# Performance work log

Hardware: AMD Instinct MI355X
Metric: run time of the kernel (lower is better)

Reference implementation:

```python
import jax, jax.numpy as jnp
import numpy as np

D = 256; NH = 8; NL = 4; NP = 4; DH = D // NH; DFFN = 1024; NQ = 900; BS = 4
SPATIAL = ((92, 92), (46, 46), (23, 23), (12, 12))  # (H, W) per level
LEVEL_START = (0, 8464, 10580, 11109)
S = sum(h * w for h, w in SPATIAL)  # 11253


def _ln(x, g, b):
    m = jnp.mean(x, -1, keepdims=True)
    v = jnp.var(x, -1, keepdims=True)
    return (x - m) / jnp.sqrt(v + 1e-5) * g + b


def setup_inputs() -> dict:
    key = jax.random.key(0)
    ks = jax.random.split(key, 24)
    p = lambda k, s: 0.02 * jax.random.normal(k, s, jnp.float32)
    return {
        "tgt": jax.random.normal(ks[0], (NQ, BS, D), jnp.float32),
        "tgt_query_pos": jax.random.normal(ks[1], (NQ, BS, D), jnp.float32),
        "tgt_reference_points": jax.random.uniform(ks[2], (NQ, BS, NL, 2), jnp.float32),
        "memory": jax.random.normal(ks[3], (S, BS, D), jnp.float32),
        "memory_spatial_shapes": jnp.array(SPATIAL, jnp.int32),
        "memory_level_start_index": jnp.array(LEVEL_START, jnp.int32),
        "in_proj_w": p(ks[4], (3 * D, D)), "in_proj_b": p(ks[5], (3 * D,)),
        "out_proj_w": p(ks[6], (D, D)), "out_proj_b": p(ks[7], (D,)),
        "off_w": p(ks[8], (NH * NL * NP * 2, D)), "off_b": p(ks[9], (NH * NL * NP * 2,)),
        "aw_w": p(ks[10], (NH * NL * NP, D)), "aw_b": p(ks[11], (NH * NL * NP,)),
        "vproj_w": p(ks[12], (D, D)), "vproj_b": p(ks[13], (D,)),
        "oproj_w": p(ks[14], (D, D)), "oproj_b": p(ks[15], (D,)),
        "ln1_g": jnp.ones((D,), jnp.float32), "ln1_b": jnp.zeros((D,), jnp.float32),
        "ln2_g": jnp.ones((D,), jnp.float32), "ln2_b": jnp.zeros((D,), jnp.float32),
        "ln3_g": jnp.ones((D,), jnp.float32), "ln3_b": jnp.zeros((D,), jnp.float32),
        "lin1_w": p(ks[16], (DFFN, D)), "lin1_b": p(ks[17], (DFFN,)),
        "lin2_w": p(ks[18], (D, DFFN)), "lin2_b": p(ks[19], (D,)),
    }


def _self_attn(q, k, v, in_w, in_b, out_w, out_b):
    # q, k, v: (nq, bs, d) -- torch nn.MultiheadAttention, eval mode
    wq, wk, wv = jnp.split(in_w, 3, axis=0)
    bq, bk, bv = jnp.split(in_b, 3)
    qp = (q @ wq.T + bq).reshape(NQ, BS, NH, DH)
    kp = (k @ wk.T + bk).reshape(NQ, BS, NH, DH)
    vp = (v @ wv.T + bv).reshape(NQ, BS, NH, DH)
    s = jnp.einsum("qbhd,kbhd->bhqk", qp, kp) / jnp.sqrt(jnp.float32(DH))
    a = jax.nn.softmax(s, axis=-1)
    o = jnp.einsum("bhqk,kbhd->qbhd", a, vp).reshape(NQ, BS, D)
    return o @ out_w.T + out_b


def _msdeform(x, ref, mem, off_w, off_b, aw_w, aw_b, vproj_w, vproj_b, oproj_w, oproj_b):
    # x: (bs, nq, d); ref: (bs, nq, nl, 2) in [0,1]; mem: (bs, S, d)
    value = (mem @ vproj_w.T + vproj_b).reshape(BS, S, NH, DH)
    off = (x @ off_w.T + off_b).reshape(BS, NQ, NH, NL, NP, 2)
    aw = jax.nn.softmax((x @ aw_w.T + aw_b).reshape(BS, NQ, NH, NL * NP), axis=-1)
    aw = aw.reshape(BS, NQ, NH, NL, NP)
    # offset normalizer = (W, H) per level
    norm = jnp.array([[w, h] for (h, w) in SPATIAL], jnp.float32)
    loc = ref[:, :, None, :, None, :] + off / norm[None, None, None, :, None, :]
    out = jnp.zeros((BS, NH, NQ, DH), x.dtype)
    for l, (H, W) in enumerate(SPATIAL):
        s0 = LEVEL_START[l]
        v = value[:, s0:s0 + H * W].transpose(0, 2, 1, 3)  # (bs, nh, H*W, dh)
        g = loc[:, :, :, l].transpose(0, 2, 1, 3, 4)       # (bs, nh, nq, np, 2)
        # grid_sample align_corners=False, padding_mode='zeros'
        px = g[..., 0] * W - 0.5
        py = g[..., 1] * H - 0.5
        x0 = jnp.floor(px).astype(jnp.int32)
        y0 = jnp.floor(py).astype(jnp.int32)
        wx = px - x0
        wy = py - y0
        samp = jnp.zeros((BS, NH, NQ, NP, DH), x.dtype)
        for dx, dy, w in ((0, 0, (1 - wx) * (1 - wy)), (1, 0, wx * (1 - wy)),
                          (0, 1, (1 - wx) * wy), (1, 1, wx * wy)):
            xi = x0 + dx
            yi = y0 + dy
            valid = ((xi >= 0) & (xi < W) & (yi >= 0) & (yi < H)).astype(x.dtype)
            idx = (jnp.clip(yi, 0, H - 1) * W + jnp.clip(xi, 0, W - 1)).reshape(BS, NH, NQ * NP)
            gat = jnp.take_along_axis(v, idx[..., None], axis=2).reshape(BS, NH, NQ, NP, DH)
            samp = samp + (w * valid)[..., None] * gat
        a = aw[:, :, :, l].transpose(0, 2, 1, 3)  # (bs, nh, nq, np)
        out = out + (samp * a[..., None]).sum(axis=3)
    out = out.transpose(0, 2, 1, 3).reshape(BS, NQ, D)
    return out @ oproj_w.T + oproj_b


def reference(tgt, tgt_query_pos, tgt_reference_points, memory,
              memory_spatial_shapes, memory_level_start_index,
              in_proj_w, in_proj_b, out_proj_w, out_proj_b,
              off_w, off_b, aw_w, aw_b, vproj_w, vproj_b, oproj_w, oproj_b,
              ln1_g, ln1_b, ln2_g, ln2_b, ln3_g, ln3_b,
              lin1_w, lin1_b, lin2_w, lin2_b):
    # module_seq = ['sa', 'ca', 'ffn']; dropout inactive (eval)
    q = tgt + tgt_query_pos
    tgt2 = _self_attn(q, q, tgt, in_proj_w, in_proj_b, out_proj_w, out_proj_b)
    tgt = _ln(tgt + tgt2, ln2_g, ln2_b)
    x = (tgt + tgt_query_pos).transpose(1, 0, 2)
    ref = tgt_reference_points.transpose(1, 0, 2, 3)
    mem = memory.transpose(1, 0, 2)
    tgt2 = _msdeform(x, ref, mem, off_w, off_b, aw_w, aw_b,
                     vproj_w, vproj_b, oproj_w, oproj_b).transpose(1, 0, 2)
    tgt = _ln(tgt + tgt2, ln1_g, ln1_b)
    ff = jax.nn.relu(tgt @ lin1_w.T + lin1_b) @ lin2_w.T + lin2_b
    return _ln(tgt + ff, ln3_g, ln3_b)
```

## Files before the change

### kernel.cpp

```cpp
#include <hip/hip_runtime.h>
#include <math.h>

#define D_MODEL 256
#define NHEAD   8
#define NLVL    4
#define NPTS    4
#define DHEAD   32
#define DFFN    1024
#define NQ      900
#define BSZ     4
#define NROW    (NQ * BSZ)
#define S_TOT   11253
#define VROWS   (S_TOT * BSZ)
#define SASCALE 0.17677669529663687f

typedef __attribute__((ext_vector_type(8))) short short8;
typedef __attribute__((ext_vector_type(4))) float f32x4;
typedef unsigned short ushort_t;

static __device__ __forceinline__ unsigned f2bf1(float f) {
    unsigned u = __float_as_uint(f);
    return (u + 0x7FFFu + ((u >> 16) & 1u)) >> 16;
}
static __device__ __forceinline__ unsigned pack2bf(float x, float y) {
// ... 243 lines not shown
                    const ushort_t* src = &Cs[r * 136 + ch];
                    uint4* dst = (uint4*)(value16 + (size_t)m * 256 + half * 128 + ch);
#pragma unroll
                    for (int j = 0; j < 4; ++j)
                        dst[j] = *(const uint4*)(src + j * 8);
                }
            }
        }
    }
}

__global__ __launch_bounds__(256) void sa_flash16(
    const ushort_t* __restrict__ qkv, ushort_t* __restrict__ attn_out)
{
    __shared__ ushort_t Ks[2 * 2080];
    __shared__ ushort_t Vt[2 * 2304];
    __shared__ ushort_t Ps[4 * 1152];

    const int t    = threadIdx.x;
    const int q0   = blockIdx.x * 64;
    const int b    = blockIdx.y & 3;
    const int h    = blockIdx.y >> 2;
    const int wv   = t >> 6;
    const int ln   = t & 63;
    const int L    = ln & 15;
    const int quad = ln >> 4;

    union { uint4 u; short8 s; } qu;
    qu.u = make_uint4(0u, 0u, 0u, 0u);
    {
        int q = q0 + wv * 16 + L;
        if (q < NQ)
            qu.u = *(const uint4*)(qkv + ((size_t)q * 4 + b) * 768 + h * 32 + quad * 8);
    }
    const short8 qf = qu.s;

    float mrun = -1e30f, lrun = 0.f;
    f32x4 oacc[2] = {{0.f,0.f,0.f,0.f},{0.f,0.f,0.f,0.f}};

    const int skey = t >> 2;
    const int sdg  = t & 3;

    uint4 ku, vu;
    auto kv_load = [&](int k0) {
        int kg = k0 + skey;
        ku = make_uint4(0u, 0u, 0u, 0u);
        vu = make_uint4(0u, 0u, 0u, 0u);
        if (kg < NQ) {
            const ushort_t* base = qkv + ((size_t)kg * 4 + b) * 768 + 256 + h * 32 + sdg * 8;
            ku = *(const uint4*)base;
            vu = *(const uint4*)(base + 256);
        }
    };

    kv_load(0);
    int it = 0;
    for (int k0 = 0; k0 < NQ; k0 += 64, it ^= 1) {
        *(uint4*)&Ks[it * 2080 + sdg * 520 + skey * 8] = ku;
        {
            ushort_t* vp = &Vt[it * 2304 + sdg * 8 * 72 + skey];
            vp[0 * 72] = (ushort_t)(vu.x & 0xffffu);
            vp[1 * 72] = (ushort_t)(vu.x >> 16);
            vp[2 * 72] = (ushort_t)(vu.y & 0xffffu);
            vp[3 * 72] = (ushort_t)(vu.y >> 16);
            vp[4 * 72] = (ushort_t)(vu.z & 0xffffu);
            vp[5 * 72] = (ushort_t)(vu.z >> 16);
            vp[6 * 72] = (ushort_t)(vu.w & 0xffffu);
            vp[7 * 72] = (ushort_t)(vu.w >> 16);
        }
        __syncthreads();
        if (k0 + 64 < NQ) kv_load(k0 + 64);

        f32x4 sacc[4] = {{0.f,0.f,0.f,0.f},{0.f,0.f,0.f,0.f},
                         {0.f,0.f,0.f,0.f},{0.f,0.f,0.f,0.f}};
#pragma unroll
        for (int cb = 0; cb < 4; ++cb) {
            short8 kf = *(const short8*)&Ks[it * 2080 + quad * 520 + (cb * 16 + L) * 8];
            sacc[cb] = __builtin_amdgcn_mfma_f32_16x16x32_bf16(kf, qf, sacc[cb], 0, 0, 0);
        }
        if (k0 + 64 > NQ) {
#pragma unroll
            for (int cb = 0; cb < 4; ++cb)
#pragma unroll
                for (int i = 0; i < 4; ++i)
                    if (k0 + cb * 16 + quad * 4 + i >= NQ) sacc[cb][i] = -1e30f;
        }

        float ml = -1e30f;
#pragma unroll
        for (int cb = 0; cb < 4; ++cb)
#pragma unroll
            for (int i = 0; i < 4; ++i) ml = fmaxf(ml, sacc[cb][i]);
        ml = fmaxf(ml, __shfl_xor(ml, 16, 64));
        ml = fmaxf(ml, __shfl_xor(ml, 32, 64));
        float mnew  = fmaxf(mrun, ml);
        float alpha = __expf(mrun - mnew);
        float p[16];
        float rs = 0.f;
#pragma unroll
        for (int cb = 0; cb < 4; ++cb)
#pragma unroll
            for (int i = 0; i < 4; ++i) {
                float e = __expf(sacc[cb][i] - mnew);
                p[cb * 4 + i] = e;
                rs += e;
            }
        rs += __shfl_xor(rs, 16, 64);
        rs += __shfl_xor(rs, 32, 64);
        lrun = lrun * alpha + rs;
        mrun = mnew;

        {
            ushort_t* pw = &Ps[wv * 1152 + L * 72];
#pragma unroll
            for (int cb = 0; cb < 4; ++cb) {
                uint2 u;
                u.x = pack2bf(p[cb * 4 + 0], p[cb * 4 + 1]);
                u.y = pack2bf(p[cb * 4 + 2], p[cb * 4 + 3]);
                *(uint2*)&pw[cb * 16 + quad * 4] = u;
            }
        }
#pragma unroll
        for (int i = 0; i < 4; ++i) {
            float ai = __shfl(alpha, quad * 4 + i, 64);
            oacc[0][i] *= ai;
            oacc[1][i] *= ai;
        }
        __syncthreads();

#pragma unroll
        for (int ks = 0; ks < 2; ++ks) {
            short8 pf = *(const short8*)&Ps[wv * 1152 + L * 72 + ks * 32 + quad * 8];
#pragma unroll
            for (int db = 0; db < 2; ++db) {
                short8 vf = *(const short8*)&Vt[it * 2304 + (db * 16 + L) * 72 + ks * 32 + quad * 8];
                oacc[db] = __builtin_amdgcn_mfma_f32_16x16x32_bf16(pf, vf, oacc[db], 0, 0, 0);
            }
        }
    }

#pragma unroll
    for (int i = 0; i < 4; ++i) {
        float lq = __shfl(lrun, quad * 4 + i, 64);
        float li = 1.f / lq;
        int q = q0 + wv * 16 + quad * 4 + i;
        if (q < NQ) {
            ushort_t* op = attn_out + ((size_t)q * 4 + b) * 256 + h * 32 + L;
            op[0]  = (ushort_t)f2bf1(oacc[0][i] * li);
            op[16] = (ushort_t)f2bf1(oacc[1][i] * li);
        }
    }
}

__global__ __launch_bounds__(256) void gemm_ln16(
    const ushort_t* __restrict__ A, const ushort_t* __restrict__ W,
    const float* __restrict__ bias, const float* __restrict__ resid,
    const float* __restrict__ gam, const float* __restrict__ bet,
    float* __restrict__ out, const float* __restrict__ pos,
    ushort_t* __restrict__ out2, int M, int K)
{
    __shared__ ushort_t As[16 * GPAD];
    __shared__ ushort_t Ws[256 * 64];
    __shared__ float sS[4][16];
    __shared__ float s2S[4][16];

    const int t  = threadIdx.x;
    const int m0 = blockIdx.x * 16;
    const int wv   = t >> 6;
    const int ln   = t & 63;
    const int L    = ln & 15;
    const int quad = ln >> 4;
    const int swz  = (L & 7) << 3;
    const int lrow = ln >> 3;
    const int lchk = (ln & 7) << 3;

    f32x4 acc[4] = {{0.f,0.f,0.f,0.f},{0.f,0.f,0.f,0.f},
                    {0.f,0.f,0.f,0.f},{0.f,0.f,0.f,0.f}};

    for (int k0 = 0; k0 < K; k0 += 64) {
#pragma unroll
        for (int j = 0; j < 8; ++j) {
            int r0 = (wv * 8 + j) * 8;
            const ushort_t* g = W + (size_t)(r0 + lrow) * K + k0 + lchk;
            stage_w16(g, &Ws[r0 * 64], ln);
        }
        if (t < 128) {
            int r = t >> 3, seg = (t & 7) * 8;
            int m = m0 + r;
            uint4 a = make_uint4(0u, 0u, 0u, 0u);
            if (m < M) a = *(const uint4*)(A + (size_t)m * K + k0 + seg);
            *(uint4*)&As[r * GPAD + seg] = a;
        }
        __syncthreads();
#pragma unroll
        for (int kh = 0; kh < 2; ++kh) {
            short8 af = *(const short8*)&As[L * GPAD + kh * 32 + quad * 8];
#pragma unroll
            for (int cb = 0; cb < 4; ++cb) {
                short8 bf = *(const short8*)&Ws[(wv * 64 + cb * 16 + L) * 64 + ((kh * 32 + quad * 8) ^ swz)];
                acc[cb] = __builtin_amdgcn_mfma_f32_16x16x32_bf16(af, bf, acc[cb], 0, 0, 0);
            }
        }
        __syncthreads();
    }

    float s[4]  = {0.f, 0.f, 0.f, 0.f};
    float s2[4] = {0.f, 0.f, 0.f, 0.f};
#pragma unroll
    for (int cb = 0; cb < 4; ++cb) {
        int col = wv * 64 + cb * 16 + L;
        float bv = bias[col];
#pragma unroll
        for (int i = 0; i < 4; ++i) {
            int m = m0 + quad * 4 + i;
            float r = (m < M) ? resid[(size_t)m * 256 + col] : 0.f;
            float xv = acc[cb][i] + bv + r;
            acc[cb][i] = xv;
            s[i]  += xv;
            s2[i] += xv * xv;
        }
    }
#pragma unroll
    for (int off = 1; off < 16; off <<= 1) {
#pragma unroll
        for (int i = 0; i < 4; ++i) {
            s[i]  += __shfl_xor(s[i],  off, 64);
            s2[i] += __shfl_xor(s2[i], off, 64);
        }
    }
    if (L == 0) {
#pragma unroll
        for (int i = 0; i < 4; ++i) {
            sS[wv][quad * 4 + i]  = s[i];
            s2S[wv][quad * 4 + i] = s2[i];
        }
    }
    __syncthreads();
    float mean[4], rstd[4];
#pragma unroll
    for (int i = 0; i < 4; ++i) {
        int row = quad * 4 + i;
        float St  = sS[0][row]  + sS[1][row]  + sS[2][row]  + sS[3][row];
        float S2t = s2S[0][row] + s2S[1][row] + s2S[2][row] + s2S[3][row];
        mean[i] = St * (1.f / 256.f);
        float var = S2t * (1.f / 256.f) - mean[i] * mean[i];
        rstd[i] = rsqrtf(var + 1e-5f);
    }
#pragma unroll
    for (int cb = 0; cb < 4; ++cb) {
        int col = wv * 64 + cb * 16 + L;
        float gv = gam[col];
        float bt = bet[col];
#pragma unroll
        for (int i = 0; i < 4; ++i) {
            int m = m0 + quad * 4 + i;
            if (m < M) {
                float y = (acc[cb][i] - mean[i]) * rstd[i] * gv + bt;
                out[(size_t)m * 256 + col] = y;
                if (out2) {
                    float o2 = y + (pos ? pos[(size_t)m * 256 + col] : 0.f);
                    out2[(size_t)m * 256 + col] = (ushort_t)f2bf1(o2);
                }
            }
        }
    }
}

__global__ __launch_bounds__(256) void offaw16(
    const ushort_t* __restrict__ A,
    const ushort_t* __restrict__ off_wb, const float* __restrict__ off_b,
    const ushort_t* __restrict__ aw_wb, const float* __restrict__ aw_b,
    float* __restrict__ off_raw, float* __restrict__ aw_raw)
{
    __shared__ ushort_t As[64 * GPAD];
    __shared__ ushort_t Ws[64 * 64];

    const int t  = threadIdx.x;
    const int m0 = blockIdx.x * 64;
    const int by = blockIdx.y;
    const bool isaw = (by >= 4);
    const int n0 = isaw ? (by - 4) * 64 : by * 64;
    const ushort_t* W = isaw ? aw_wb : off_wb;
    const float* bs = isaw ? aw_b : off_b;
    float* C = isaw ? aw_raw : off_raw;
    const int ldc = isaw ? 128 : 256;

    const int trow = t >> 2;
    const int tk   = (t & 3) << 4;
    const int wv   = t >> 6;
    const int ln   = t & 63;
    const int L    = ln & 15;
    const int quad = ln >> 4;
    const int swz  = (L & 7) << 3;
    const int lrow = ln >> 3;
    const int lchk = (ln & 7) << 3;

    const int  mrow = m0 + trow;
    const bool mv   = (mrow < NROW);
    const ushort_t* arow = A + (size_t)mrow * 256 + tk;

    f32x4 acc[4] = {{0.f,0.f,0.f,0.f},{0.f,0.f,0.f,0.f},
                    {0.f,0.f,0.f,0.f},{0.f,0.f,0.f,0.f}};

    for (int k0 = 0; k0 < 256; k0 += 64) {
#pragma unroll
        for (int j = 0; j < 2; ++j) {
            int r0 = (wv * 2 + j) * 8;
            const ushort_t* g = W + (size_t)(n0 + r0 + lrow) * 256 + k0 + lchk;
            stage_w16(g, &Ws[r0 * 64], ln);
        }
        {
            uint4 a0 = make_uint4(0u,0u,0u,0u), a1 = a0;
            if (mv) {
                a0 = *(const uint4*)(arow + k0);
                a1 = *(const uint4*)(arow + k0 + 8);
            }
            *(uint4*)&As[trow * GPAD + tk + 0] = a0;
            *(uint4*)&As[trow * GPAD + tk + 8] = a1;
        }
        __syncthreads();
#pragma unroll
        for (int kh = 0; kh < 2; ++kh) {
            short8 af = *(const short8*)&As[(wv * 16 + L) * GPAD + kh * 32 + quad * 8];
#pragma unroll
            for (int cb = 0; cb < 4; ++cb) {
                short8 bf = *(const short8*)&Ws[(cb * 16 + L) * 64 + ((kh * 32 + quad * 8) ^ swz)];
                acc[cb] = __builtin_amdgcn_mfma_f32_16x16x32_bf16(af, bf, acc[cb], 0, 0, 0);
            }
        }
        __syncthreads();
    }
#pragma unroll
    for (int cb = 0; cb < 4; ++cb) {
        int col = n0 + cb * 16 + L;
        float bv = bs[col];
#pragma unroll
        for (int i = 0; i < 4; ++i) {
            int m = m0 + wv * 16 + quad * 4 + i;
            if (m < NROW)
                C[(size_t)m * ldc + col] = acc[cb][i] + bv;
        }
    }
}

__global__ __launch_bounds__(256) void gemm16_16(
    const ushort_t* __restrict__ A, const ushort_t* __restrict__ W,
    const float* __restrict__ bias, ushort_t* __restrict__ C,
    int M, int N, int K, int ldc, int relu)
{
    __shared__ ushort_t As[64 * GPAD];
    __shared__ ushort_t Ws[64 * 64];

    const int t  = threadIdx.x;
    const int m0 = blockIdx.x * 64;
    const int n0 = blockIdx.y * 64;
    const int trow = t >> 2;
    const int tk   = (t & 3) << 4;
    const int wv   = t >> 6;
    const int ln   = t & 63;
    const int L    = ln & 15;
    const int quad = ln >> 4;
    const int swz  = (L & 7) << 3;
    const int lrow = ln >> 3;
    const int lchk = (ln & 7) << 3;

    const int  mrow = m0 + trow;
    const bool mv   = (mrow < M);
    const ushort_t* arow = A + (size_t)mrow * K + tk;

    f32x4 acc[4] = {{0.f,0.f,0.f,0.f},{0.f,0.f,0.f,0.f},
                    {0.f,0.f,0.f,0.f},{0.f,0.f,0.f,0.f}};

    for (int k0 = 0; k0 < K; k0 += 64) {
#pragma unroll
        for (int j = 0; j < 2; ++j) {
            int r0 = (wv * 2 + j) * 8;
            const ushort_t* g = W + (size_t)(n0 + r0 + lrow) * K + k0 + lchk;
            stage_w16(g, &Ws[r0 * 64], ln);
        }
        {
            uint4 a0 = make_uint4(0u,0u,0u,0u), a1 = a0;
            if (mv) {
                a0 = *(const uint4*)(arow + k0);
                a1 = *(const uint4*)(arow + k0 + 8);
            }
            *(uint4*)&As[trow * GPAD + tk + 0] = a0;
            *(uint4*)&As[trow * GPAD + tk + 8] = a1;
        }
        __syncthreads();
#pragma unroll
        for (int kh = 0; kh < 2; ++kh) {
            short8 af = *(const short8*)&As[(wv * 16 + L) * GPAD + kh * 32 + quad * 8];
#pragma unroll
            for (int cb = 0; cb < 4; ++cb) {
                short8 bf = *(const short8*)&Ws[(cb * 16 + L) * 64 + ((kh * 32 + quad * 8) ^ swz)];
                acc[cb] = __builtin_amdgcn_mfma_f32_16x16x32_bf16(af, bf, acc[cb], 0, 0, 0);
            }
        }
        __syncthreads();
    }
#pragma unroll
    for (int cb = 0; cb < 4; ++cb) {
        int col = n0 + cb * 16 + L;
        float bv = bias[col];
#pragma unroll
        for (int i = 0; i < 4; ++i) {
            int m = m0 + wv * 16 + quad * 4 + i;
            if (m < M) {
                float o = acc[cb][i] + bv;
                if (relu) o = fmaxf(o, 0.f);
                C[(size_t)m * ldc + col] = (ushort_t)f2bf1(o);
            }
        }
    }
}

__global__ __launch_bounds__(256) void msdeform16(
    const float* __restrict__ off_raw, const float* __restrict__ aw_raw,
    const float* __restrict__ refp, const ushort_t* __restrict__ value,
    ushort_t* __restrict__ out)
{
    const int row = blockIdx.x;
    const int b = row & 3;
    const int t = threadIdx.x;

    __shared__ float aw_s[8][17];
    __shared__ float px_s[8][16];
    __shared__ float py_s[8][16];

    const int Hs[4]  = {92, 46, 23, 12};
    const int Wd[4]  = {92, 46, 23, 12};
    const int S0_[4] = {0, 8464, 10580, 11109};

    if (t < 128) {
        int hh = t >> 4, lp = t & 15, l = lp >> 2;
        float ox = off_raw[(size_t)row * 256 + hh * 32 + lp * 2 + 0];
        float oy = off_raw[(size_t)row * 256 + hh * 32 + lp * 2 + 1];
        float rx = refp[((size_t)row * 4 + l) * 2 + 0];
        float ry = refp[((size_t)row * 4 + l) * 2 + 1];
        px_s[hh][lp] = rx * (float)Wd[l] + ox - 0.5f;
        py_s[hh][lp] = ry * (float)Hs[l] + oy - 0.5f;
    }
    if (t < 8) {
        int hh = t;
        float v[16];
        float m = -1e30f;
#pragma unroll
        for (int j = 0; j < 16; ++j) {
            v[j] = aw_raw[(size_t)row * 128 + hh * 16 + j];
            m = fmaxf(m, v[j]);
        }
        float ssum = 0.f;
#pragma unroll
        for (int j = 0; j < 16; ++j) { v[j] = __expf(v[j] - m); ssum += v[j]; }
        float inv = 1.f / ssum;
#pragma unroll
        for (int j = 0; j < 16; ++j) aw_s[hh][j] = v[j] * inv;
    }
    __syncthreads();

    const int h = t >> 5, d = t & 31;
    const ushort_t* vb = value + (size_t)b * 256 + h * 32 + d;
    float acc = 0.f;
#pragma unroll
    for (int l = 0; l < 4; ++l) {
        const int H = Hs[l], W = Wd[l], base = S0_[l];
#pragma unroll
        for (int p = 0; p < 4; ++p) {
            const int lp = l * 4 + p;
            float px = px_s[h][lp], py = py_s[h][lp];
            float x0f = floorf(px), y0f = floorf(py);
            int x0 = (int)x0f, y0 = (int)y0f;
            float wx = px - x0f, wy = py - y0f;
            float sv = 0.f;
#pragma unroll
            for (int dy = 0; dy < 2; ++dy) {
#pragma unroll
                for (int dx = 0; dx < 2; ++dx) {
                    int xi = x0 + dx, yi = y0 + dy;
                    float flag = (xi >= 0 && xi < W && yi >= 0 && yi < H) ? 1.f : 0.f;
                    int xc = xi < 0 ? 0 : (xi >= W ? W - 1 : xi);
                    int yc = yi < 0 ? 0 : (yi >= H ? H - 1 : yi);
                    float wgt = (dx ? wx : 1.f - wx) * (dy ? wy : 1.f - wy);
                    float gv = bf2f(vb[(size_t)(base + yc * W + xc) * 1024]);
                    sv = fmaf(wgt * flag, gv, sv);
                }
            }
            acc = fmaf(aw_s[h][lp], sv, acc);
        }
    }
    out[(size_t)row * 256 + h * 32 + d] = (ushort_t)f2bf1(acc);
}

extern "C" void kernel_launch(void* const* d_in, const int* in_sizes, int n_in,
                              void* d_out, int out_size, void* d_ws, size_t ws_size,
                              hipStream_t stream)
{
    const float* tgt    = (const float*)d_in[0];
    const float* qpos   = (const float*)d_in[1];
    const float* refp   = (const float*)d_in[2];
    const float* mem    = (const float*)d_in[3];
    const float* in_w   = (const float*)d_in[6];
    const float* in_b   = (const float*)d_in[7];
    const float* outp_w = (const float*)d_in[8];
    const float* outp_b = (const float*)d_in[9];
    const float* off_w  = (const float*)d_in[10];
    const float* off_b  = (const float*)d_in[11];
    const float* aw_w   = (const float*)d_in[12];
    const float* aw_b   = (const float*)d_in[13];
    const float* vp_w   = (const float*)d_in[14];
    const float* vp_b   = (const float*)d_in[15];
    const float* op_w   = (const float*)d_in[16];
    const float* op_b   = (const float*)d_in[17];
    const float* ln1g   = (const float*)d_in[18];
    const float* ln1b   = (const float*)d_in[19];
    const float* ln2g   = (const float*)d_in[20];
    const float* ln2b   = (const float*)d_in[21];
    const float* ln3g   = (const float*)d_in[22];
    const float* ln3b   = (const float*)d_in[23];
    const float* l1w    = (const float*)d_in[24];
    const float* l1b    = (const float*)d_in[25];
    const float* l2w    = (const float*)d_in[26];
    const float* l2b    = (const float*)d_in[27];
    float* out = (float*)d_out;
    float* ws  = (float*)d_ws;

    ushort_t* qkv16    = (ushort_t*)ws;
    ushort_t* att16    = (ushort_t*)(ws + 691200);
    float*    tgt_a    = ws + 1843200;
    ushort_t* xca16    = (ushort_t*)(ws + 2764800);
    float*    off_raw  = ws + 2995200;
    float*    aw_raw   = ws + 3916800;
    ushort_t* att2_16  = (ushort_t*)(ws + 4377600);
    float*    tgt_b    = ws + 4608000;
    ushort_t* tgtb16   = (ushort_t*)(ws + 5529600);
    ushort_t* value16  = (ushort_t*)(ws + 5760000);
    ushort_t* hidden16 = (ushort_t*)(ws + 11521536);
    ushort_t* wb       = (ushort_t*)(ws + 13364736);

    const ushort_t* in_wb   = wb + WB_IN;
    const ushort_t* vp_wb   = wb + WB_VP;
    const ushort_t* outp_wb = wb + WB_OUTP;
    const ushort_t* off_wb  = wb + WB_OFF;
    const ushort_t* aw_wb   = wb + WB_AW;
    const ushort_t* op_wb   = wb + WB_OP;
    const ushort_t* l1_wb   = wb + WB_L1;
    const ushort_t* l2_wb   = wb + WB_L2;

    dim3 b256(256);

    hipLaunchKernelGGL(cvt_weights, dim3(496), b256, 0, stream,
                       in_w, vp_w, outp_w, off_w, aw_w, op_w, l1w, l2w, wb);
    hipLaunchKernelGGL(proj_fused, dim3(1388), b256, 0, stream,
                       tgt, qpos, in_wb, in_b, mem, vp_wb, vp_b, qkv16, value16);
    hipLaunchKernelGGL(sa_flash16, dim3(15, 32), b256, 0, stream, qkv16, att16);
    hipLaunchKernelGGL(gemm_ln16, dim3(225), b256, 0, stream,
                       att16, outp_wb, outp_b, tgt, ln2g, ln2b,
                       tgt_a, qpos, xca16, NROW, 256);
    hipLaunchKernelGGL(offaw16, dim3(57, 6), b256, 0, stream,
                       xca16, off_wb, off_b, aw_wb, aw_b, off_raw, aw_raw);
    hipLaunchKernelGGL(msdeform16, dim3(3600), b256, 0, stream,
                       off_raw, aw_raw, refp, value16, att2_16);
    hipLaunchKernelGGL(gemm_ln16, dim3(225), b256, 0, stream,
                       att2_16, op_wb, op_b, tgt_a, ln1g, ln1b,
                       tgt_b, (const float*)nullptr, tgtb16, NROW, 256);
    hipLaunchKernelGGL(gemm16_16, dim3(57, 16), b256, 0, stream,
                       tgtb16, l1_wb, l1b, hidden16, NROW, 1024, 256, 1024, 1);
    hipLaunchKernelGGL(gemm_ln16, dim3(225), b256, 0, stream,
                       hidden16, l2_wb, l2b, tgt_b, ln3g, ln3b,
                       out, (const float*)nullptr, (ushort_t*)nullptr, NROW, 1024);
}
```

Baseline: 267.0 us.

## Fuse post-attention tail into one per-row-tile megakernel with LDS intermediates

Replaces six launches (out-proj+LN, offset/attention-weight GEMMs, deformable sampling, op-proj+LN, FFN lin1, lin2+LN) with a single 512-thread kernel per 16-row tile. All intermediates stay in shared memory, and the FFN hidden layer is produced and consumed in 256-wide chunks. This removes global round trips and launch gaps. In exchange only 225 blocks run with heavy LDS use at one block per CU. Every block re-streams all weights, and the sampling phase has less parallelism per block, so GEMM efficiency and occupancy may drop.

```diff
diff --git a/kernel.cpp b/kernel.cpp
--- a/kernel.cpp
+++ b/kernel.cpp
@@ -419,20 +419,35 @@
     }
 }
 
-__global__ __launch_bounds__(256) void gemm_ln16(
-    const ushort_t* __restrict__ A, const ushort_t* __restrict__ W,
-    const float* __restrict__ bias, const float* __restrict__ resid,
-    const float* __restrict__ gam, const float* __restrict__ bet,
-    float* __restrict__ out, const float* __restrict__ pos,
-    ushort_t* __restrict__ out2, int M, int K)
+__global__ __launch_bounds__(512, 1) void tail_fused(
+    const ushort_t* __restrict__ att16,
+    const float* __restrict__ tgt, const float* __restrict__ qpos,
+    const ushort_t* __restrict__ outp_wb, const float* __restrict__ outp_b,
+    const float* __restrict__ ln2g, const float* __restrict__ ln2b,
+    const ushort_t* __restrict__ off_wb, const float* __restrict__ off_b,
+    const ushort_t* __restrict__ aw_wb, const float* __restrict__ aw_b,
+    const float* __restrict__ refp, const ushort_t* __restrict__ value16,
+    const ushort_t* __restrict__ op_wb, const float* __restrict__ op_b,
+    const float* __restrict__ ln1g, const float* __restrict__ ln1b,
+    const ushort_t* __restrict__ l1_wb, const float* __restrict__ l1b,
+    const ushort_t* __restrict__ l2_wb, const float* __restrict__ l2b,
+    const float* __restrict__ ln3g, const float* __restrict__ ln3b,
+    float* __restrict__ out)
 {
+    __shared__ ushort_t Ws[256 * 64];
     __shared__ ushort_t As[16 * GPAD];
-    __shared__ ushort_t Ws[256 * 64];
-    __shared__ float sS[4][16];
-    __shared__ float s2S[4][16];
-
-    const int t  = threadIdx.x;
-    const int m0 = blockIdx.x * 16;
+    __shared__ ushort_t xca_s[16 * 264];
+    __shared__ ushort_t att2_s[16 * 264];
+    __shared__ ushort_t tgtb16_s[16 * 264];
+    __shared__ float    tgta_s[16 * 256];
+    __shared__ float    tgtb_s[16 * 256];
+    __shared__ float    pxs[16 * 128];
+    __shared__ float    pys[16 * 128];
+    __shared__ float    aws[16 * 128];
+    __shared__ float    sS[8][16], s2S[8][16];
+
+    const int t    = threadIdx.x;
+    const int m0   = blockIdx.x * 16;
     const int wv   = t >> 6;
     const int ln   = t & 63;
     const int L    = ln & 15;
@@ -440,323 +455,328 @@
     const int swz  = (L & 7) << 3;
     const int lrow = ln >> 3;
     const int lchk = (ln & 7) << 3;
-
-    f32x4 acc[4] = {{0.f,0.f,0.f,0.f},{0.f,0.f,0.f,0.f},
-                    {0.f,0.f,0.f,0.f},{0.f,0.f,0.f,0.f}};
-
-    for (int k0 = 0; k0 < K; k0 += 64) {
-#pragma unroll
-        for (int j = 0; j < 8; ++j) {
-            int r0 = (wv * 8 + j) * 8;
-            const ushort_t* g = W + (size_t)(r0 + lrow) * K + k0 + lchk;
+    const int rloc = quad * 4;
+
+    auto stageW256 = [&](const ushort_t* Wb, int rowoff, int kstride, int koff) {
+#pragma unroll
+        for (int j = 0; j < 4; ++j) {
+            int r0 = (wv * 4 + j) * 8;
+            const ushort_t* g = Wb + (size_t)(rowoff + r0 + lrow) * kstride + koff + lchk;
             stage_w16(g, &Ws[r0 * 64], ln);
         }
+    };
+    auto mfma2 = [&](const ushort_t* Alds, int astride, int ak0, f32x4* acc) {
+#pragma unroll
+        for (int kh = 0; kh < 2; ++kh) {
+            short8 af = *(const short8*)&Alds[L * astride + ak0 + kh * 32 + quad * 8];
+#pragma unroll
+            for (int cb = 0; cb < 2; ++cb) {
+                short8 bf = *(const short8*)&Ws[(wv * 32 + cb * 16 + L) * 64 + ((kh * 32 + quad * 8) ^ swz)];
+                acc[cb] = __builtin_amdgcn_mfma_f32_16x16x32_bf16(af, bf, acc[cb], 0, 0, 0);
+            }
+        }
+    };
+
+    {
+        f32x4 acc[2] = {{0.f,0.f,0.f,0.f},{0.f,0.f,0.f,0.f}};
+        for (int k0 = 0; k0 < 256; k0 += 64) {
+            stageW256(outp_wb, 0, 256, k0);
+            if (t < 128) {
+                int r = t >> 3, seg = (t & 7) * 8;
+                uint4 a = *(const uint4*)(att16 + (size_t)(m0 + r) * 256 + k0 + seg);
+                *(uint4*)&As[r * GPAD + seg] = a;
+            }
+            __syncthreads();
+            mfma2(As, GPAD, 0, acc);
+            __syncthreads();
+        }
+        float s[4] = {0.f,0.f,0.f,0.f}, s2v[4] = {0.f,0.f,0.f,0.f};
+#pragma unroll
+        for (int cb = 0; cb < 2; ++cb) {
+            int col = wv * 32 + cb * 16 + L;
+            float bv = outp_b[col];
+#pragma unroll
+            for (int i = 0; i < 4; ++i) {
+                float xv = acc[cb][i] + bv + tgt[(size_t)(m0 + rloc + i) * 256 + col];
+                acc[cb][i] = xv;
+                s[i] += xv; s2v[i] += xv * xv;
+            }
+        }
+#pragma unroll
+        for (int off = 1; off < 16; off <<= 1)
+#pragma unroll
+            for (int i = 0; i < 4; ++i) {
+                s[i]  += __shfl_xor(s[i],  off, 64);
+                s2v[i] += __shfl_xor(s2v[i], off, 64);
+            }
+        if (L == 0)
+#pragma unroll
+            for (int i = 0; i < 4; ++i) { sS[wv][rloc + i] = s[i]; s2S[wv][rloc + i] = s2v[i]; }
+        __syncthreads();
+        float mean[4], rstd[4];
+#pragma unroll
+        for (int i = 0; i < 4; ++i) {
+            float St = 0.f, S2t = 0.f;
+#pragma unroll
+            for (int w = 0; w < 8; ++w) { St += sS[w][rloc + i]; S2t += s2S[w][rloc + i]; }
+            mean[i] = St * (1.f / 256.f);
+            float var = S2t * (1.f / 256.f) - mean[i] * mean[i];
+            rstd[i] = rsqrtf(var + 1e-5f);
+        }
+#pragma unroll
+        for (int cb = 0; cb < 2; ++cb) {
+            int col = wv * 32 + cb * 16 + L;
+            float gv = ln2g[col], bt = ln2b[col];
+#pragma unroll
+            for (int i = 0; i < 4; ++i) {
+                float y = (acc[cb][i] - mean[i]) * rstd[i] * gv + bt;
+                tgta_s[(rloc + i) * 256 + col] = y;
+                xca_s[(rloc + i) * 264 + col] =
+                    (ushort_t)f2bf1(y + qpos[(size_t)(m0 + rloc + i) * 256 + col]);
+            }
+        }
+        __syncthreads();
+    }
+
+    const float Hs[4] = {92.f, 46.f, 23.f, 12.f};
+    const int   HsI[4] = {92, 46, 23, 12};
+    const int   S0_[4] = {0, 8464, 10580, 11109};
+
+    {
+        f32x4 acc[2] = {{0.f,0.f,0.f,0.f},{0.f,0.f,0.f,0.f}};
+        for (int k0 = 0; k0 < 256; k0 += 64) {
+            stageW256(off_wb, 0, 256, k0);
+            __syncthreads();
+            mfma2(xca_s, 264, k0, acc);
+            __syncthreads();
+        }
+#pragma unroll
+        for (int cb = 0; cb < 2; ++cb) {
+            int col = wv * 32 + cb * 16 + L;
+            float bv = off_b[col];
+            int hh = col >> 5, lp = (col & 31) >> 1, isY = col & 1;
+            int l = lp >> 2;
+            float dim = Hs[l];
+            float* dst = isY ? pys : pxs;
+#pragma unroll
+            for (int i = 0; i < 4; ++i) {
+                float ref = refp[((size_t)(m0 + rloc + i) * 4 + l) * 2 + isY];
+                dst[(rloc + i) * 128 + hh * 16 + lp] = ref * dim + (acc[cb][i] + bv) - 0.5f;
+            }
+        }
+    }
+
+    {
+        f32x4 acc = {0.f,0.f,0.f,0.f};
+        for (int k0 = 0; k0 < 256; k0 += 64) {
+            __syncthreads();
+#pragma unroll
+            for (int j = 0; j < 2; ++j) {
+                int r0 = (wv * 2 + j) * 8;
+                const ushort_t* g = aw_wb + (size_t)(r0 + lrow) * 256 + k0 + lchk;
+                stage_w16(g, &Ws[r0 * 64], ln);
+            }
+            __syncthreads();
+#pragma unroll
+            for (int kh = 0; kh < 2; ++kh) {
+                short8 af = *(const short8*)&xca_s[L * 264 + k0 + kh * 32 + quad * 8];
+                short8 bf = *(const short8*)&Ws[(wv * 16 + L) * 64 + ((kh * 32 + quad * 8) ^ swz)];
+                acc = __builtin_amdgcn_mfma_f32_16x16x32_bf16(af, bf, acc, 0, 0, 0);
+            }
+        }
+        __syncthreads();
+        {
+            int col = wv * 16 + L;
+            float bv = aw_b[col];
+#pragma unroll
+            for (int i = 0; i < 4; ++i)
+                aws[(rloc + i) * 128 + col] = acc[i] + bv;
+        }
+        __syncthreads();
         if (t < 128) {
-            int r = t >> 3, seg = (t & 7) * 8;
-            int m = m0 + r;
-            uint4 a = make_uint4(0u, 0u, 0u, 0u);
-            if (m < M) a = *(const uint4*)(A + (size_t)m * K + k0 + seg);
-            *(uint4*)&As[r * GPAD + seg] = a;
-        }
-        __syncthreads();
-#pragma unroll
-        for (int kh = 0; kh < 2; ++kh) {
-            short8 af = *(const short8*)&As[L * GPAD + kh * 32 + quad * 8];
-#pragma unroll
-            for (int cb = 0; cb < 4; ++cb) {
-                short8 bf = *(const short8*)&Ws[(wv * 64 + cb * 16 + L) * 64 + ((kh * 32 + quad * 8) ^ swz)];
-                acc[cb] = __builtin_amdgcn_mfma_f32_16x16x32_bf16(af, bf, acc[cb], 0, 0, 0);
-            }
-        }
-        __syncthreads();
-    }
-
-    float s[4]  = {0.f, 0.f, 0.f, 0.f};
-    float s2[4] = {0.f, 0.f, 0.f, 0.f};
-#pragma unroll
-    for (int cb = 0; cb < 4; ++cb) {
-        int col = wv * 64 + cb * 16 + L;
-        float bv = bias[col];
+            int r = t >> 3, hh = t & 7;
+            float v[16];
+            float m = -1e30f;
+#pragma unroll
+            for (int j = 0; j < 16; ++j) { v[j] = aws[r * 128 + hh * 16 + j]; m = fmaxf(m, v[j]); }
+            float ssum = 0.f;
+#pragma unroll
+            for (int j = 0; j < 16; ++j) { v[j] = __expf(v[j] - m); ssum += v[j]; }
+            float inv = 1.f / ssum;
+#pragma unroll
+            for (int j = 0; j < 16; ++j) aws[r * 128 + hh * 16 + j] = v[j] * inv;
+        }
+        __syncthreads();
+    }
+
+    {
+        const int h2 = (t >> 5) & 7, d2 = t & 31, r2 = t >> 8;
+#pragma unroll 2
+        for (int rp = 0; rp < 8; ++rp) {
+            int row = rp * 2 + r2;
+            int b = (m0 + row) & 3;
+            const ushort_t* vb = value16 + (size_t)b * 256 + h2 * 32 + d2;
+            float accv = 0.f;
+#pragma unroll
+            for (int l = 0; l < 4; ++l) {
+                const int H = HsI[l], W = HsI[l], base = S0_[l];
+#pragma unroll
+                for (int p = 0; p < 4; ++p) {
+                    const int lp = l * 4 + p;
+                    float px = pxs[row * 128 + h2 * 16 + lp];
+                    float py = pys[row * 128 + h2 * 16 + lp];
+                    float x0f = floorf(px), y0f = floorf(py);
+                    int x0 = (int)x0f, y0 = (int)y0f;
+                    float wx = px - x0f, wy = py - y0f;
+                    float sv = 0.f;
+#pragma unroll
+                    for (int dy = 0; dy < 2; ++dy)
+#pragma unroll
+                        for (int dx = 0; dx < 2; ++dx) {
+                            int xi = x0 + dx, yi = y0 + dy;
+                            float flag = (xi >= 0 && xi < W && yi >= 0 && yi < H) ? 1.f : 0.f;
+                            int xc = xi < 0 ? 0 : (xi >= W ? W - 1 : xi);
+                            int yc = yi < 0 ? 0 : (yi >= H ? H - 1 : yi);
+                            float wgt = (dx ? wx : 1.f - wx) * (dy ? wy : 1.f - wy);
+                            float gv = bf2f(vb[(size_t)(base + yc * W + xc) * 1024]);
+                            sv = fmaf(wgt * flag, gv, sv);
+                        }
+                    accv = fmaf(aws[row * 128 + h2 * 16 + lp], sv, accv);
+                }
+            }
+            att2_s[row * 264 + h2 * 32 + d2] = (ushort_t)f2bf1(accv);
+        }
+        __syncthreads();
+    }
+
+    {
+        f32x4 acc[2] = {{0.f,0.f,0.f,0.f},{0.f,0.f,0.f,0.f}};
+        for (int k0 = 0; k0 < 256; k0 += 64) {
+            stageW256(op_wb, 0, 256, k0);
+            __syncthreads();
+            mfma2(att2_s, 264, k0, acc);
+            __syncthreads();
+        }
+        float s[4] = {0.f,0.f,0.f,0.f}, s2v[4] = {0.f,0.f,0.f,0.f};
+#pragma unroll
+        for (int cb = 0; cb < 2; ++cb) {
+            int col = wv * 32 + cb * 16 + L;
+            float bv = op_b[col];
+#pragma unroll
+            for (int i = 0; i < 4; ++i) {
+                float xv = acc[cb][i] + bv + tgta_s[(rloc + i) * 256 + col];
+                acc[cb][i] = xv;
+                s[i] += xv; s2v[i] += xv * xv;
+            }
+        }
+#pragma unroll
+        for (int off = 1; off < 16; off <<= 1)
+#pragma unroll
+            for (int i = 0; i < 4; ++i) {
+                s[i]  += __shfl_xor(s[i],  off, 64);
+                s2v[i] += __shfl_xor(s2v[i], off, 64);
+            }
+        if (L == 0)
+#pragma unroll
+            for (int i = 0; i < 4; ++i) { sS[wv][rloc + i] = s[i]; s2S[wv][rloc + i] = s2v[i]; }
+        __syncthreads();
+        float mean[4], rstd[4];
 #pragma unroll
         for (int i = 0; i < 4; ++i) {
-            int m = m0 + quad * 4 + i;
-            float r = (m < M) ? resid[(size_t)m * 256 + col] : 0.f;
-            float xv = acc[cb][i] + bv + r;
-            acc[cb][i] = xv;
-            s[i]  += xv;
-            s2[i] += xv * xv;
-        }
-    }
-#pragma unroll
-    for (int off = 1; off < 16; off <<= 1) {
+            float St = 0.f, S2t = 0.f;
+#pragma unroll
+            for (int w = 0; w < 8; ++w) { St += sS[w][rloc + i]; S2t += s2S[w][rloc + i]; }
+            mean[i] = St * (1.f / 256.f);
+            float var = S2t * (1.f / 256.f) - mean[i] * mean[i];
+            rstd[i] = rsqrtf(var + 1e-5f);
+        }
+#pragma unroll
+        for (int cb = 0; cb < 2; ++cb) {
+            int col = wv * 32 + cb * 16 + L;
+            float gv = ln1g[col], bt = ln1b[col];
+#pragma unroll
+            for (int i = 0; i < 4; ++i) {
+                float y = (acc[cb][i] - mean[i]) * rstd[i] * gv + bt;
+                tgtb_s[(rloc + i) * 256 + col] = y;
+                tgtb16_s[(rloc + i) * 264 + col] = (ushort_t)f2bf1(y);
+            }
+        }
+        __syncthreads();
+    }
+
+    {
+        f32x4 accf[2] = {{0.f,0.f,0.f,0.f},{0.f,0.f,0.f,0.f}};
+        ushort_t* hc = att2_s;
+        for (int c = 0; c < 4; ++c) {
+            f32x4 acch[2] = {{0.f,0.f,0.f,0.f},{0.f,0.f,0.f,0.f}};
+            for (int k0 = 0; k0 < 256; k0 += 64) {
+                stageW256(l1_wb, c * 256, 256, k0);
+                __syncthreads();
+                mfma2(tgtb16_s, 264, k0, acch);
+                __syncthreads();
+            }
+#pragma unroll
+            for (int cb = 0; cb < 2; ++cb) {
+                int colc = wv * 32 + cb * 16 + L;
+                float bv = l1b[c * 256 + colc];
+#pragma unroll
+                for (int i = 0; i < 4; ++i) {
+                    float hv = fmaxf(acch[cb][i] + bv, 0.f);
+                    hc[(rloc + i) * 264 + colc] = (ushort_t)f2bf1(hv);
+                }
+            }
+            __syncthreads();
+            for (int k0 = 0; k0 < 256; k0 += 64) {
+                stageW256(l2_wb, 0, 1024, c * 256 + k0);
+                __syncthreads();
+                mfma2(hc, 264, k0, accf);
+                __syncthreads();
+            }
+        }
+        float s[4] = {0.f,0.f,0.f,0.f}, s2v[4] = {0.f,0.f,0.f,0.f};
+#pragma unroll
+        for (int cb = 0; cb < 2; ++cb) {
+            int col = wv * 32 + cb * 16 + L;
+            float bv = l2b[col];
+#pragma unroll
+            for (int i = 0; i < 4; ++i) {
+                float xv = accf[cb][i] + bv + tgtb_s[(rloc + i) * 256 + col];
+                accf[cb][i] = xv;
+                s[i] += xv; s2v[i] += xv * xv;
+            }
+        }
+#pragma unroll
+        for (int off = 1; off < 16; off <<= 1)
+#pragma unroll
+            for (int i = 0; i < 4; ++i) {
+                s[i]  += __shfl_xor(s[i],  off, 64);
+                s2v[i] += __shfl_xor(s2v[i], off, 64);
+            }
+        if (L == 0)
+#pragma unroll
+            for (int i = 0; i < 4; ++i) { sS[wv][rloc + i] = s[i]; s2S[wv][rloc + i] = s2v[i]; }
+        __syncthreads();
+        float mean[4], rstd[4];
 #pragma unroll
         for (int i = 0; i < 4; ++i) {
-            s[i]  += __shfl_xor(s[i],  off, 64);
-            s2[i] += __shfl_xor(s2[i], off, 64);
-        }
-    }
-    if (L == 0) {
-#pragma unroll
-        for (int i = 0; i < 4; ++i) {
-            sS[wv][quad * 4 + i]  = s[i];
-            s2S[wv][quad * 4 + i] = s2[i];
-        }
-    }
-    __syncthreads();
-    float mean[4], rstd[4];
-#pragma unroll
-    for (int i = 0; i < 4; ++i) {
-        int row = quad * 4 + i;
-        float St  = sS[0][row]  + sS[1][row]  + sS[2][row]  + sS[3][row];
-        float S2t = s2S[0][row] + s2S[1][row] + s2S[2][row] + s2S[3][row];
-        mean[i] = St * (1.f / 256.f);
-        float var = S2t * (1.f / 256.f) - mean[i] * mean[i];
-        rstd[i] = rsqrtf(var + 1e-5f);
-    }
-#pragma unroll
-    for (int cb = 0; cb < 4; ++cb) {
-        int col = wv * 64 + cb * 16 + L;
-        float gv = gam[col];
-        float bt = bet[col];
-#pragma unroll
-        for (int i = 0; i < 4; ++i) {
-            int m = m0 + quad * 4 + i;
-            if (m < M) {
-                float y = (acc[cb][i] - mean[i]) * rstd[i] * gv + bt;
-                out[(size_t)m * 256 + col] = y;
-                if (out2) {
-                    float o2 = y + (pos ? pos[(size_t)m * 256 + col] : 0.f);
-                    out2[(size_t)m * 256 + col] = (ushort_t)f2bf1(o2);
-                }
-            }
-        }
-    }
-}
-
-__global__ __launch_bounds__(256) void offaw16(
-    const ushort_t* __restrict__ A,
-    const ushort_t* __restrict__ off_wb, const float* __restrict__ off_b,
-    const ushort_t* __restrict__ aw_wb, const float* __restrict__ aw_b,
-    float* __restrict__ off_raw, float* __restrict__ aw_raw)
-{
-    __shared__ ushort_t As[64 * GPAD];
-    __shared__ ushort_t Ws[64 * 64];
-
-    const int t  = threadIdx.x;
-    const int m0 = blockIdx.x * 64;
-    const int by = blockIdx.y;
-    const bool isaw = (by >= 4);
-    const int n0 = isaw ? (by - 4) * 64 : by * 64;
-    const ushort_t* W = isaw ? aw_wb : off_wb;
-    const float* bs = isaw ? aw_b : off_b;
-    float* C = isaw ? aw_raw : off_raw;
-    const int ldc = isaw ? 128 : 256;
-
-    const int trow = t >> 2;
-    const int tk   = (t & 3) << 4;
-    const int wv   = t >> 6;
-    const int ln   = t & 63;
-    const int L    = ln & 15;
-    const int quad = ln >> 4;
-    const int swz  = (L & 7) << 3;
-    const int lrow = ln >> 3;
-    const int lchk = (ln & 7) << 3;
-
-    const int  mrow = m0 + trow;
-    const bool mv   = (mrow < NROW);
-    const ushort_t* arow = A + (size_t)mrow * 256 + tk;
-
-    f32x4 acc[4] = {{0.f,0.f,0.f,0.f},{0.f,0.f,0.f,0.f},
-                    {0.f,0.f,0.f,0.f},{0.f,0.f,0.f,0.f}};
-
-    for (int k0 = 0; k0 < 256; k0 += 64) {
-#pragma unroll
-        for (int j = 0; j < 2; ++j) {
-            int r0 = (wv * 2 + j) * 8;
-            const ushort_t* g = W + (size_t)(n0 + r0 + lrow) * 256 + k0 + lchk;
-            stage_w16(g, &Ws[r0 * 64], ln);
-        }
-        {
-            uint4 a0 = make_uint4(0u,0u,0u,0u), a1 = a0;
-            if (mv) {
-                a0 = *(const uint4*)(arow + k0);
-                a1 = *(const uint4*)(arow + k0 + 8);
-            }
-            *(uint4*)&As[trow * GPAD + tk + 0] = a0;
-            *(uint4*)&As[trow * GPAD + tk + 8] = a1;
-        }
-        __syncthreads();
-#pragma unroll
-        for (int kh = 0; kh < 2; ++kh) {
-            short8 af = *(const short8*)&As[(wv * 16 + L) * GPAD + kh * 32 + quad * 8];
-#pragma unroll
-            for (int cb = 0; cb < 4; ++cb) {
-                short8 bf = *(const short8*)&Ws[(cb * 16 + L) * 64 + ((kh * 32 + quad * 8) ^ swz)];
-                acc[cb] = __builtin_amdgcn_mfma_f32_16x16x32_bf16(af, bf, acc[cb], 0, 0, 0);
-            }
-        }
-        __syncthreads();
-    }
-#pragma unroll
-    for (int cb = 0; cb < 4; ++cb) {
-        int col = n0 + cb * 16 + L;
-        float bv = bs[col];
-#pragma unroll
-        for (int i = 0; i < 4; ++i) {
-            int m = m0 + wv * 16 + quad * 4 + i;
-            if (m < NROW)
-                C[(size_t)m * ldc + col] = acc[cb][i] + bv;
-        }
-    }
-}
-
-__global__ __launch_bounds__(256) void gemm16_16(
-    const ushort_t* __restrict__ A, const ushort_t* __restrict__ W,
-    const float* __restrict__ bias, ushort_t* __restrict__ C,
-    int M, int N, int K, int ldc, int relu)
-{
-    __shared__ ushort_t As[64 * GPAD];
-    __shared__ ushort_t Ws[64 * 64];
-
-    const int t  = threadIdx.x;
-    const int m0 = blockIdx.x * 64;
-    const int n0 = blockIdx.y * 64;
-    const int trow = t >> 2;
-    const int tk   = (t & 3) << 4;
-    const int wv   = t >> 6;
-    const int ln   = t & 63;
-    const int L    = ln & 15;
-    const int quad = ln >> 4;
-    const int swz  = (L & 7) << 3;
-    const int lrow = ln >> 3;
-    const int lchk = (ln & 7) << 3;
-
-    const int  mrow = m0 + trow;
-    const bool mv   = (mrow < M);
-    const ushort_t* arow = A + (size_t)mrow * K + tk;
-
-    f32x4 acc[4] = {{0.f,0.f,0.f,0.f},{0.f,0.f,0.f,0.f},
-                    {0.f,0.f,0.f,0.f},{0.f,0.f,0.f,0.f}};
-
-    for (int k0 = 0; k0 < K; k0 += 64) {
-#pragma unroll
-        for (int j = 0; j < 2; ++j) {
-            int r0 = (wv * 2 + j) * 8;
-            const ushort_t* g = W + (size_t)(n0 + r0 + lrow) * K + k0 + lchk;
-            stage_w16(g, &Ws[r0 * 64], ln);
-        }
-        {
-            uint4 a0 = make_uint4(0u,0u,0u,0u), a1 = a0;
-            if (mv) {
-                a0 = *(const uint4*)(arow + k0);
-                a1 = *(const uint4*)(arow + k0 + 8);
-            }
-            *(uint4*)&As[trow * GPAD + tk + 0] = a0;
-            *(uint4*)&As[trow * GPAD + tk + 8] = a1;
-        }
-        __syncthreads();
-#pragma unroll
-        for (int kh = 0; kh < 2; ++kh) {
-            short8 af = *(const short8*)&As[(wv * 16 + L) * GPAD + kh * 32 + quad * 8];
-#pragma unroll
-            for (int cb = 0; cb < 4; ++cb) {
-                short8 bf = *(const short8*)&Ws[(cb * 16 + L) * 64 + ((kh * 32 + quad * 8) ^ swz)];
-                acc[cb] = __builtin_amdgcn_mfma_f32_16x16x32_bf16(af, bf, acc[cb], 0, 0, 0);
-            }
-        }
-        __syncthreads();
-    }
-#pragma unroll
-    for (int cb = 0; cb < 4; ++cb) {
-        int col = n0 + cb * 16 + L;
-        float bv = bias[col];
-#pragma unroll
-        for (int i = 0; i < 4; ++i) {
-            int m = m0 + wv * 16 + quad * 4 + i;
-            if (m < M) {
-                float o = acc[cb][i] + bv;
-                if (relu) o = fmaxf(o, 0.f);
-                C[(size_t)m * ldc + col] = (ushort_t)f2bf1(o);
-            }
-        }
-    }
-}
-
-__global__ __launch_bounds__(256) void msdeform16(
-    const float* __restrict__ off_raw, const float* __restrict__ aw_raw,
-    const float* __restrict__ refp, const ushort_t* __restrict__ value,
-    ushort_t* __restrict__ out)
-{
-    const int row = blockIdx.x;
-    const int b = row & 3;
-    const int t = threadIdx.x;
-
-    __shared__ float aw_s[8][17];
-    __shared__ float px_s[8][16];
-    __shared__ float py_s[8][16];
-
-    const int Hs[4]  = {92, 46, 23, 12};
-    const int Wd[4]  = {92, 46, 23, 12};
-    const int S0_[4] = {0, 8464, 10580, 11109};
-
-    if (t < 128) {
-        int hh = t >> 4, lp = t & 15, l = lp >> 2;
-        float ox = off_raw[(size_t)row * 256 + hh * 32 + lp * 2 + 0];
-        float oy = off_raw[(size_t)row * 256 + hh * 32 + lp * 2 + 1];
-        float rx = refp[((size_t)row * 4 + l) * 2 + 0];
-        float ry = refp[((size_t)row * 4 + l) * 2 + 1];
-        px_s[hh][lp] = rx * (float)Wd[l] + ox - 0.5f;
-        py_s[hh][lp] = ry * (float)Hs[l] + oy - 0.5f;
-    }
-    if (t < 8) {
-        int hh = t;
-        float v[16];
-        float m = -1e30f;
-#pragma unroll
-        for (int j = 0; j < 16; ++j) {
-            v[j] = aw_raw[(size_t)row * 128 + hh * 16 + j];
-            m = fmaxf(m, v[j]);
-        }
-        float ssum = 0.f;
-#pragma unroll
-        for (int j = 0; j < 16; ++j) { v[j] = __expf(v[j] - m); ssum += v[j]; }
-        float inv = 1.f / ssum;
-#pragma unroll
-        for (int j = 0; j < 16; ++j) aw_s[hh][j] = v[j] * inv;
-    }
-    __syncthreads();
-
-    const int h = t >> 5, d = t & 31;
-    const ushort_t* vb = value + (size_t)b * 256 + h * 32 + d;
-    float acc = 0.f;
-#pragma unroll
-    for (int l = 0; l < 4; ++l) {
-        const int H = Hs[l], W = Wd[l], base = S0_[l];
-#pragma unroll
-        for (int p = 0; p < 4; ++p) {
-            const int lp = l * 4 + p;
-            float px = px_s[h][lp], py = py_s[h][lp];
-            float x0f = floorf(px), y0f = floorf(py);
-            int x0 = (int)x0f, y0 = (int)y0f;
-            float wx = px - x0f, wy = py - y0f;
-            float sv = 0.f;
-#pragma unroll
-            for (int dy = 0; dy < 2; ++dy) {
-#pragma unroll
-                for (int dx = 0; dx < 2; ++dx) {
-                    int xi = x0 + dx, yi = y0 + dy;
-                    float flag = (xi >= 0 && xi < W && yi >= 0 && yi < H) ? 1.f : 0.f;
-                    int xc = xi < 0 ? 0 : (xi >= W ? W - 1 : xi);
-                    int yc = yi < 0 ? 0 : (yi >= H ? H - 1 : yi);
-                    float wgt = (dx ? wx : 1.f - wx) * (dy ? wy : 1.f - wy);
-                    float gv = bf2f(vb[(size_t)(base + yc * W + xc) * 1024]);
-                    sv = fmaf(wgt * flag, gv, sv);
-                }
-            }
-            acc = fmaf(aw_s[h][lp], sv, acc);
-        }
-    }
-    out[(size_t)row * 256 + h * 32 + d] = (ushort_t)f2bf1(acc);
+            float St = 0.f, S2t = 0.f;
+#pragma unroll
+            for (int w = 0; w < 8; ++w) { St += sS[w][rloc + i]; S2t += s2S[w][rloc + i]; }
+            mean[i] = St * (1.f / 256.f);
+            float var = S2t * (1.f / 256.f) - mean[i] * mean[i];
+            rstd[i] = rsqrtf(var + 1e-5f);
+        }
+#pragma unroll
+        for (int cb = 0; cb < 2; ++cb) {
+            int col = wv * 32 + cb * 16 + L;
+            float gv = ln3g[col], bt = ln3b[col];
+#pragma unroll
+            for (int i = 0; i < 4; ++i) {
+                float y = (accf[cb][i] - mean[i]) * rstd[i] * gv + bt;
+                out[(size_t)(m0 + rloc + i) * 256 + col] = y;
+            }
+        }
+    }
 }
 
 extern "C" void kernel_launch(void* const* d_in, const int* in_sizes, int n_in,
@@ -794,15 +814,7 @@
 
     ushort_t* qkv16    = (ushort_t*)ws;
     ushort_t* att16    = (ushort_t*)(ws + 691200);
-    float*    tgt_a    = ws + 1843200;
-    ushort_t* xca16    = (ushort_t*)(ws + 2764800);
-    float*    off_raw  = ws + 2995200;
-    float*    aw_raw   = ws + 3916800;
-    ushort_t* att2_16  = (ushort_t*)(ws + 4377600);
-    float*    tgt_b    = ws + 4608000;
-    ushort_t* tgtb16   = (ushort_t*)(ws + 5529600);
     ushort_t* value16  = (ushort_t*)(ws + 5760000);
-    ushort_t* hidden16 = (ushort_t*)(ws + 11521536);
     ushort_t* wb       = (ushort_t*)(ws + 13364736);
 
     const ushort_t* in_wb   = wb + WB_IN;
@@ -821,19 +833,12 @@
     hipLaunchKernelGGL(proj_fused, dim3(1388), b256, 0, stream,
                        tgt, qpos, in_wb, in_b, mem, vp_wb, vp_b, qkv16, value16);
     hipLaunchKernelGGL(sa_flash16, dim3(15, 32), b256, 0, stream, qkv16, att16);
-    hipLaunchKernelGGL(gemm_ln16, dim3(225), b256, 0, stream,
-                       att16, outp_wb, outp_b, tgt, ln2g, ln2b,
-                       tgt_a, qpos, xca16, NROW, 256);
-    hipLaunchKernelGGL(offaw16, dim3(57, 6), b256, 0, stream,
-                       xca16, off_wb, off_b, aw_wb, aw_b, off_raw, aw_raw);
-    hipLaunchKernelGGL(msdeform16, dim3(3600), b256, 0, stream,
-                       off_raw, aw_raw, refp, value16, att2_16);
-    hipLaunchKernelGGL(gemm_ln16, dim3(225), b256, 0, stream,
-                       att2_16, op_wb, op_b, tgt_a, ln1g, ln1b,
-                       tgt_b, (const float*)nullptr, tgtb16, NROW, 256);
-    hipLaunchKernelGGL(gemm16_16, dim3(57, 16), b256, 0, stream,
-                       tgtb16, l1_wb, l1b, hidden16, NROW, 1024, 256, 1024, 1);
-    hipLaunchKernelGGL(gemm_ln16, dim3(225), b256, 0, stream,
-                       hidden16, l2_wb, l2b, tgt_b, ln3g, ln3b,
-                       out, (const float*)nullptr, (ushort_t*)nullptr, NROW, 1024);
+    hipLaunchKernelGGL(tail_fused, dim3(225), dim3(512), 0, stream,
+                       att16, tgt, qpos,
+                       outp_wb, outp_b, ln2g, ln2b,
+                       off_wb, off_b, aw_wb, aw_b,
+                       refp, value16,
+                       op_wb, op_b, ln1g, ln1b,
+                       l1_wb, l1b, l2_wb, l2b,
+                       ln3g, ln3b, out);
 }
```

Measured after the change: 308.1 us. +15.4%, slower.
